# Kernel tuning notes

Measured on AMD Instinct MI355X. Metric: run time of the kernel, lower is better.

## Reference

```python
import jax, jax.numpy as jnp
import numpy as np

HEAD_NUM = 16
ROPE_BASE = 10000.0


def _rotate_half(x):
    # interleaved pairs: (x0,x1,x2,x3,...) -> (-x1,x0,-x3,x2,...)
    x_even = x[..., ::2]
    x_odd = x[..., 1::2]
    return jnp.stack((-x_odd, x_even), axis=-1).reshape(x.shape)


def _rope_cos_sin(seq_len, head_dim):
    half = head_dim // 2
    inv_freq = 1.0 / (ROPE_BASE ** (jnp.arange(half, dtype=jnp.float32) / half))
    t = jnp.arange(seq_len, dtype=jnp.float32)
    freqs = t[:, None] * inv_freq[None, :]            # [S, half]
    cos = jnp.repeat(jnp.cos(freqs), 2, axis=-1)       # [S, D]
    sin = jnp.repeat(jnp.sin(freqs), 2, axis=-1)       # [S, D]
    return cos, sin


def setup_inputs() -> dict:
    key = jax.random.key(0)
    ks = jax.random.split(key, 9)
    B, S, H = 2, 2048, 2048
    std = 1.0 / np.sqrt(H)
    return {
        "x": jax.random.normal(ks[0], (B, S, H), jnp.float32),
        "Wq": jax.random.normal(ks[1], (H, H), jnp.float32) * std,
        "bq": jax.random.normal(ks[2], (H,), jnp.float32) * std,
        "Wk": jax.random.normal(ks[3], (H, H), jnp.float32) * std,
        "bk": jax.random.normal(ks[4], (H,), jnp.float32) * std,
        "Wv": jax.random.normal(ks[5], (H, H), jnp.float32) * std,
        "bv": jax.random.normal(ks[6], (H,), jnp.float32) * std,
        "Wo": jax.random.normal(ks[7], (H, H), jnp.float32) * std,
        "bo": jax.random.normal(ks[8], (H,), jnp.float32) * std,
    }


def reference(x, Wq, bq, Wk, bk, Wv, bv, Wo, bo):
    B, S, H = x.shape
    nh = HEAD_NUM
    d = H // nh
    scale = jnp.float32(np.sqrt(d))

    def proj(W, b):
        y = x @ W.T + b                                 # torch Linear: x W^T + b
        return y.reshape(B, S, nh, d).transpose(0, 2, 1, 3)  # [B, nh, S, d]

    Q = proj(Wq, bq)
    K = proj(Wk, bk)
    V = proj(Wv, bv)

    cos, sin = _rope_cos_sin(S, d)                      # [S, d]
    Q = Q * cos + _rotate_half(Q) * sin
    K = K * cos + _rotate_half(K) * sin

    scores = jnp.einsum("bhqd,bhkd->bhqk", Q, K) / scale  # [B, nh, S, S]
    causal = jnp.tril(jnp.ones((S, S), dtype=bool))
    scores = jnp.where(causal, scores, jnp.float32(-jnp.inf))
    attn = jax.nn.softmax(scores, axis=-1)
    out = jnp.einsum("bhqk,bhkd->bhqd", attn, V)        # [B, nh, S, d]
    out = out.transpose(0, 2, 1, 3).reshape(B, S, H)
    return out @ Wo.T + bo
```

## Files before the change

kernel.cpp:

```cpp
#include <hip/hip_runtime.h>
#include <math.h>

typedef __bf16 bf16x8 __attribute__((ext_vector_type(8)));
typedef float floatx4 __attribute__((ext_vector_type(4)));

__device__ __forceinline__ unsigned short f32_to_bf16(float f) {
  unsigned int u = __float_as_uint(f);
  u = u + 0x7FFFu + ((u >> 16) & 1u);
  return (unsigned short)(u >> 16);
}
__device__ __forceinline__ float bf16_to_f32(unsigned short s) {
  return __uint_as_float(((unsigned int)s) << 16);
}

__device__ __forceinline__ void gld_lds16(const unsigned short* g,
                                          unsigned short* l) {
  __builtin_amdgcn_global_load_lds(
      (const __attribute__((address_space(1))) unsigned int*)g,
      (__attribute__((address_space(3))) unsigned int*)l, 16, 0, 0);
}

__global__ void cast_kernel(const float* __restrict__ in,
                            unsigned short* __restrict__ out, int n4) {
  int i = blockIdx.x * blockDim.x + threadIdx.x;
  if (i >= n4) return;
  const float4 v = reinterpret_cast<const float4*>(in)[i];
  ushort4 o;
  o.x = f32_to_bf16(v.x); o.y = f32_to_bf16(v.y);
  o.z = f32_to_bf16(v.z); o.w = f32_to_bf16(v.w);
  reinterpret_cast<ushort4*>(out)[i] = o;
}

__global__ void cast4_kernel(const float* __restrict__ a,
                             const float* __restrict__ b,
                             const float* __restrict__ c,
                             const float* __restrict__ d,
                             unsigned short* __restrict__ oa,
                             unsigned short* __restrict__ ob,
                             unsigned short* __restrict__ oc,
                             unsigned short* __restrict__ od, int n4) {
  int i = blockIdx.x * blockDim.x + threadIdx.x;
  if (i >= n4) return;
  const float* in;
  unsigned short* out;
  switch (blockIdx.y) {
    case 0: in = a; out = oa; break;
    case 1: in = b; out = ob; break;
    case 2: in = c; out = oc; break;
    default: in = d; out = od; break;
  }
  const float4 v = reinterpret_cast<const float4*>(in)[i];
  ushort4 o;
  o.x = f32_to_bf16(v.x); o.y = f32_to_bf16(v.y);
  o.z = f32_to_bf16(v.z); o.w = f32_to_bf16(v.w);
  reinterpret_cast<ushort4*>(out)[i] = o;
}

__global__ void rope_table_kernel(float2* __restrict__ tab, int total) {
  int idx = blockIdx.x * blockDim.x + threadIdx.x;
  if (idx >= total) return;
  const int s = idx >> 6, i = idx & 63;
  const float inv = powf(10000.0f, -(float)i * (1.0f / 64.0f));
  const float ang = (float)s * inv;
  tab[idx] = make_float2(cosf(ang), sinf(ang));
}

template <int EPI>
__global__ __launch_bounds__(256) void gemm_fused(
    const unsigned short* __restrict__ A, const unsigned short* __restrict__ B,
    const float* __restrict__ bias, float* __restrict__ Cf,
    unsigned short* __restrict__ Cb, const float2* __restrict__ tab,
    float scl, int M, int N, int K, int S) {
  __shared__ unsigned short As[128 * 64];
  __shared__ unsigned short Bs[128 * 64];
  const int t = threadIdx.x;
  const int lane = t & 63;
  const int w = t >> 6;
  const int bm = blockIdx.y * 128;
  const int bn = blockIdx.x * 128;
  const int wm = (w & 1) * 64;
  const int wn = (w >> 1) * 64;
  const int m16 = lane & 15;
  const int quad = lane >> 4;
  const int key = m16 & 7;

  const int lr = lane >> 3;
  const int lc = ((lane & 7) ^ lr) * 8;

  floatx4 acc[4][4];
#pragma unroll
  for (int i = 0; i < 4; ++i)
#pragma unroll
    for (int j = 0; j < 4; ++j) acc[i][j] = floatx4{0.f, 0.f, 0.f, 0.f};

  const unsigned short* Abase = A + (size_t)(bm + w * 32 + lr) * K + lc;
  const unsigned short* Bbase = B + (size_t)(bn + w * 32 + lr) * K + lc;

  for (int k0 = 0; k0 < K; k0 += 64) {
    __syncthreads();
#pragma unroll
    for (int it = 0; it < 4; ++it) {
      gld_lds16(Abase + (size_t)it * 8 * K + k0, &As[(w * 4 + it) * 512]);
      gld_lds16(Bbase + (size_t)it * 8 * K + k0, &Bs[(w * 4 + it) * 512]);
    }
    __syncthreads();
#pragma unroll
    for (int ks = 0; ks < 64; ks += 32) {
      const int ck = ks >> 3;
      bf16x8 af[4], bfr[4];
#pragma unroll
      for (int i = 0; i < 4; ++i)
        af[i] = *reinterpret_cast<const bf16x8*>(
            &As[(wm + i * 16 + m16) * 64 + ((ck | quad) ^ key) * 8]);
#pragma unroll
      for (int j = 0; j < 4; ++j)
        bfr[j] = *reinterpret_cast<const bf16x8*>(
            &Bs[(wn + j * 16 + m16) * 64 + ((ck | quad) ^ key) * 8]);
#pragma unroll
      for (int i = 0; i < 4; ++i)
#pragma unroll
        for (int j = 0; j < 4; ++j)
          acc[i][j] = __builtin_amdgcn_mfma_f32_16x16x32_bf16(
              af[i], bfr[j], acc[i][j], 0, 0, 0);
    }
  }

#pragma unroll
  for (int i = 0; i < 4; ++i) {
    const int rbase = bm + wm + i * 16 + quad * 4;
#pragma unroll
    for (int j = 0; j < 4; ++j) {
      const int col = bn + wn + j * 16 + m16;
      const float bvv = bias[col];
      if (EPI == 0) {
#pragma unroll
        for (int r = 0; r < 4; ++r)
          Cf[(size_t)(rbase + r) * N + col] = acc[i][j][r] + bvv;
      }
    }
  }
}

__global__ __launch_bounds__(256) void gemm_qkv(
    const unsigned short* __restrict__ A, const unsigned short* __restrict__ Bq,
    const unsigned short* __restrict__ Bk, const unsigned short* __restrict__ Bv,
    const float* __restrict__ biasq, const float* __restrict__ biask,
    const float* __restrict__ biasv, unsigned short* __restrict__ Qb,
    unsigned short* __restrict__ Kb, unsigned short* __restrict__ Vtb,
    const float2* __restrict__ tab, float qscale, int M, int N, int K, int S) {
  __shared__ unsigned short As[128 * 64];
  __shared__ unsigned short Bs[128 * 64];
  const int t = threadIdx.x;
  const int lane = t & 63;
  const int w = t >> 6;
  const int z = blockIdx.z;
  const int bm = blockIdx.y * 128;
  const int bn = blockIdx.x * 128;
  const int wm = (w & 1) * 64;
  const int wn = (w >> 1) * 64;
  const int m16 = lane & 15;
  const int quad = lane >> 4;
  const int key = m16 & 7;

  const int lr = lane >> 3;
  const int lc = ((lane & 7) ^ lr) * 8;

  const unsigned short* B = (z == 0) ? Bq : ((z == 1) ? Bk : Bv);
  const float* bias = (z == 0) ? biasq : ((z == 1) ? biask : biasv);
  unsigned short* Cb = (z == 0) ? Qb : ((z == 1) ? Kb : Vtb);
  const float scl = (z == 0) ? qscale : 1.0f;

  floatx4 acc[4][4];
#pragma unroll
  for (int i = 0; i < 4; ++i)
#pragma unroll
    for (int j = 0; j < 4; ++j) acc[i][j] = floatx4{0.f, 0.f, 0.f, 0.f};

  const unsigned short* Abase = A + (size_t)(bm + w * 32 + lr) * K + lc;
  const unsigned short* Bbase = B + (size_t)(bn + w * 32 + lr) * K + lc;

  for (int k0 = 0; k0 < K; k0 += 64) {
    __syncthreads();
#pragma unroll
    for (int it = 0; it < 4; ++it) {
      gld_lds16(Abase + (size_t)it * 8 * K + k0, &As[(w * 4 + it) * 512]);
      gld_lds16(Bbase + (size_t)it * 8 * K + k0, &Bs[(w * 4 + it) * 512]);
    }
    __syncthreads();
#pragma unroll
    for (int ks = 0; ks < 64; ks += 32) {
      const int ck = ks >> 3;
      bf16x8 af[4], bfr[4];
#pragma unroll
      for (int i = 0; i < 4; ++i)
        af[i] = *reinterpret_cast<const bf16x8*>(
            &As[(wm + i * 16 + m16) * 64 + ((ck | quad) ^ key) * 8]);
#pragma unroll
      for (int j = 0; j < 4; ++j)
        bfr[j] = *reinterpret_cast<const bf16x8*>(
            &Bs[(wn + j * 16 + m16) * 64 + ((ck | quad) ^ key) * 8]);
#pragma unroll
      for (int i = 0; i < 4; ++i)
#pragma unroll
        for (int j = 0; j < 4; ++j)
          acc[i][j] = __builtin_amdgcn_mfma_f32_16x16x32_bf16(
              af[i], bfr[j], acc[i][j], 0, 0, 0);
    }
  }

#pragma unroll
  for (int i = 0; i < 4; ++i) {
    const int rbase = bm + wm + i * 16 + quad * 4;
#pragma unroll
    for (int j = 0; j < 4; ++j) {
      const int col = bn + wn + j * 16 + m16;
      const float bvv = bias[col];
      if (z != 2) {
        const int pi = (col & 127) >> 1;
#pragma unroll
        for (int r = 0; r < 4; ++r) {
          const int row = rbase + r;
          const int s = row & (S - 1);
          const float v = acc[i][j][r] + bvv;
          const float vp = __shfl_xor(v, 1);
          const float2 cs = tab[s * 64 + pi];
          const float oe = (v * cs.x - vp * cs.y) * scl;
          const float oo = (vp * cs.x + v * cs.y) * scl;
          if ((m16 & 1) == 0) {
            const unsigned pk =
                (unsigned)f32_to_bf16(oe) | ((unsigned)f32_to_bf16(oo) << 16);
            *reinterpret_cast<unsigned*>(Cb + (size_t)row * N + col) = pk;
          }
        }
      } else {
        const int b = rbase >> 11;
        const int s = rbase & (S - 1);
        ushort4 pk;
        pk.x = f32_to_bf16(acc[i][j][0] + bvv);
        pk.y = f32_to_bf16(acc[i][j][1] + bvv);
        pk.z = f32_to_bf16(acc[i][j][2] + bvv);
        pk.w = f32_to_bf16(acc[i][j][3] + bvv);
        *reinterpret_cast<ushort4*>(
            Cb + ((size_t)((b << 11) + col)) * S + s) = pk;
      }
    }
  }
}

constexpr int F_BQ = 128, F_BK = 64, F_DH = 128;
constexpr int KS_STR = 136;
constexpr int VS_STR = 72;
constexpr int PS_STR = 72;

__global__ __launch_bounds__(256, 2) void fattn_kernel(
    const unsigned short* __restrict__ Qb, const unsigned short* __restrict__ Kb,
    const unsigned short* __restrict__ Vtb, unsigned short* __restrict__ Ob,
    int S, int H, int nh) {
  __shared__ unsigned short Ks[F_BK * KS_STR];
  __shared__ unsigned short Vts[F_DH * VS_STR];
  __shared__ unsigned short Ps[F_BQ * PS_STR];

  const int t = threadIdx.x;
  const int lane = t & 63;
  const int w = t >> 6;
  const int l15 = lane & 15;
  const int quad = lane >> 4;

  const int i = blockIdx.x;
  const int bh = i & 31;
  const int qt = (i < 256) ? (i >> 5) : (15 - ((i - 256) >> 5));
  const int h = bh & 15;
  const int b = bh >> 4;
  const int q0 = qt * F_BQ;

  const unsigned short* Qrow = Qb + ((size_t)(b * S + q0)) * H + h * F_DH;
  const unsigned short* Krow = Kb + ((size_t)b * S) * H + h * F_DH;
  const unsigned short* Vtrow = Vtb + ((size_t)bh * F_DH) * S;
  unsigned short* Orow = Ob + ((size_t)(b * S + q0)) * H + h * F_DH;

  const int kt = t >> 2, ck0 = (t & 3) * 32;
  const int vd = t >> 1, cv0 = (t & 1) * 32;
  const unsigned short* Kg = Krow + (size_t)kt * H + ck0;
  const unsigned short* Vg = Vtrow + (size_t)vd * S + cv0;

  bf16x8 aq[2][4];
#pragma unroll
  for (int qg = 0; qg < 2; ++qg)
#pragma unroll
    for (int ks = 0; ks < 4; ++ks)
      aq[qg][ks] = *reinterpret_cast<const bf16x8*>(
          Qrow + (size_t)(w * 32 + qg * 16 + l15) * H + ks * 32 + quad * 8);

  uint4 kreg[4], vreg[4];
#pragma unroll
  for (int ii = 0; ii < 4; ++ii)
    kreg[ii] = *reinterpret_cast<const uint4*>(Kg + ii * 8);
#pragma unroll
  for (int ii = 0; ii < 4; ++ii)
    vreg[ii] = *reinterpret_cast<const uint4*>(Vg + ii * 8);

  floatx4 oacc[2][8];
#pragma unroll
  for (int qg = 0; qg < 2; ++qg)
#pragma unroll
    for (int dj = 0; dj < 8; ++dj) oacc[qg][dj] = floatx4{0.f, 0.f, 0.f, 0.f};
  float lpart[2][4] = {{0.f, 0.f, 0.f, 0.f}, {0.f, 0.f, 0.f, 0.f}};
  int qrow[2][4];
#pragma unroll
  for (int qg = 0; qg < 2; ++qg)
#pragma unroll
    for (int r = 0; r < 4; ++r)
      qrow[qg][r] = q0 + w * 32 + qg * 16 + quad * 4 + r;

  const int ntile = q0 / F_BK + 2;
  for (int tile = 0; tile < ntile; ++tile) {
    const int k0 = tile * F_BK;
    __syncthreads();
#pragma unroll
    for (int ii = 0; ii < 4; ++ii)
      *reinterpret_cast<uint4*>(&Ks[kt * KS_STR + ck0 + ii * 8]) = kreg[ii];
#pragma unroll
    for (int ii = 0; ii < 4; ++ii)
      *reinterpret_cast<uint4*>(&Vts[vd * VS_STR + cv0 + ii * 8]) = vreg[ii];
    __syncthreads();

    if (tile + 1 < ntile) {
      const int k1 = (tile + 1) * F_BK;
#pragma unroll
      for (int ii = 0; ii < 4; ++ii)
        kreg[ii] = *reinterpret_cast<const uint4*>(Kg + (size_t)k1 * H + ii * 8);
#pragma unroll
      for (int ii = 0; ii < 4; ++ii)
        vreg[ii] = *reinterpret_cast<const uint4*>(Vg + k1 + ii * 8);
    }

    floatx4 sacc[2][4];
#pragma unroll
    for (int qg = 0; qg < 2; ++qg)
#pragma unroll
      for (int j = 0; j < 4; ++j) sacc[qg][j] = floatx4{0.f, 0.f, 0.f, 0.f};
#pragma unroll
    for (int j = 0; j < 4; ++j) {
      bf16x8 bk[4];
#pragma unroll
      for (int ks = 0; ks < 4; ++ks)
        bk[ks] = *reinterpret_cast<const bf16x8*>(
            &Ks[(j * 16 + l15) * KS_STR + ks * 32 + quad * 8]);
#pragma unroll
      for (int qg = 0; qg < 2; ++qg)
#pragma unroll
        for (int ks = 0; ks < 4; ++ks)
          sacc[qg][j] = __builtin_amdgcn_mfma_f32_16x16x32_bf16(
              aq[qg][ks], bk[ks], sacc[qg][j], 0, 0, 0);
    }

#pragma unroll
    for (int qg = 0; qg < 2; ++qg)
#pragma unroll
      for (int j = 0; j < 4; ++j) {
        const int ktg = k0 + j * 16 + l15;
#pragma unroll
        for (int r = 0; r < 4; ++r) {
          const float p =
              (ktg <= qrow[qg][r]) ? exp2f(sacc[qg][j][r]) : 0.0f;
          lpart[qg][r] += p;
          Ps[(w * 32 + qg * 16 + quad * 4 + r) * PS_STR + j * 16 + l15] =
              f32_to_bf16(p);
        }
      }

#pragma unroll
    for (int ks2 = 0; ks2 < 2; ++ks2) {
      bf16x8 ap[2];
#pragma unroll
      for (int qg = 0; qg < 2; ++qg)
        ap[qg] = *reinterpret_cast<const bf16x8*>(
            &Ps[(w * 32 + qg * 16 + l15) * PS_STR + ks2 * 32 + quad * 8]);
#pragma unroll
      for (int dj = 0; dj < 8; ++dj) {
        const bf16x8 bv = *reinterpret_cast<const bf16x8*>(
            &Vts[(dj * 16 + l15) * VS_STR + ks2 * 32 + quad * 8]);
#pragma unroll
        for (int qg = 0; qg < 2; ++qg)
          oacc[qg][dj] = __builtin_amdgcn_mfma_f32_16x16x32_bf16(
              ap[qg], bv, oacc[qg][dj], 0, 0, 0);
      }
    }
  }

#pragma unroll
  for (int qg = 0; qg < 2; ++qg)
#pragma unroll
    for (int r = 0; r < 4; ++r) {
      float l = lpart[qg][r];
      l += __shfl_xor(l, 1);
      l += __shfl_xor(l, 2);
      l += __shfl_xor(l, 4);
      l += __shfl_xor(l, 8);
      const float linv = 1.0f / l;
      unsigned short* orow =
          Orow + (size_t)(w * 32 + qg * 16 + quad * 4 + r) * H;
#pragma unroll
      for (int dj = 0; dj < 8; ++dj)
        orow[dj * 16 + l15] = f32_to_bf16(oacc[qg][dj][r] * linv);
    }
}

extern "C" void kernel_launch(void* const* d_in, const int* in_sizes, int n_in,
                              void* d_out, int out_size, void* d_ws,
                              size_t ws_size, hipStream_t stream) {
  const float* x  = (const float*)d_in[0];
  const float* Wq = (const float*)d_in[1];
  const float* bq = (const float*)d_in[2];
  const float* Wk = (const float*)d_in[3];
  const float* bk = (const float*)d_in[4];
  const float* Wv = (const float*)d_in[5];
  const float* bv = (const float*)d_in[6];
  const float* Wo = (const float*)d_in[7];
  const float* bo = (const float*)d_in[8];
  float* out = (float*)d_out;

  const int B = 2, S = 2048, H = 2048, nh = 16;
  const int M = B * S;

  unsigned short* Wqb = (unsigned short*)d_ws;
  unsigned short* Wkb = Wqb + (size_t)H * H;
  unsigned short* Wvb = Wkb + (size_t)H * H;
  unsigned short* Wob = Wvb + (size_t)H * H;
  unsigned short* xb  = Wob + (size_t)H * H;
  unsigned short* Qbb = xb + (size_t)M * H;
  unsigned short* Kbb = Qbb + (size_t)M * H;
  unsigned short* Vtb = Kbb + (size_t)M * H;
  unsigned short* Ob  = Vtb + (size_t)M * H;
  float2* tab = (float2*)(Ob + (size_t)M * H);

  const int cast_w4 = H * H / 4;
  const int cast_x4 = M * H / 4;
  const int tab_n = S * 64;

  rope_table_kernel<<<dim3(tab_n / 256), dim3(256), 0, stream>>>(tab, tab_n);
  cast_kernel<<<dim3(cast_x4 / 256), dim3(256), 0, stream>>>(x, xb, cast_x4);
  cast4_kernel<<<dim3(cast_w4 / 256, 4), dim3(256), 0, stream>>>(
      Wq, Wk, Wv, Wo, Wqb, Wkb, Wvb, Wob, cast_w4);

  const float qscale = 0.08838834764831845f * 1.4426950408889634f;

  gemm_qkv<<<dim3(H / 128, M / 128, 3), dim3(256), 0, stream>>>(
      xb, Wqb, Wkb, Wvb, bq, bk, bv, Qbb, Kbb, Vtb, tab, qscale, M, H, H, S);

  fattn_kernel<<<dim3((S / F_BQ) * B * nh), dim3(256), 0, stream>>>(
      Qbb, Kbb, Vtb, Ob, S, H, nh);

  gemm_fused<0><<<dim3(H / 128, M / 128), dim3(256), 0, stream>>>(
      Ob, Wob, bo, out, nullptr, nullptr, 1.0f, M, H, H, S);
}
```

Baseline: 473.3 us.

## Swizzle GEMM workgroup order and drop register prefetch in flash attention

Both GEMM kernels remap the linear workgroup id in groups of 8, interleaving blocks across a stride of nwg/8, so that concurrently running workgroups are intended to share A/B tiles in L2/MALL. The attention kernel removes the software prefetch of the next K/V tile into registers and instead loads each tile synchronously from global memory into LDS at the start of its iteration. This lowers register pressure and may allow higher occupancy, but global load latency is no longer hidden behind the MFMA work of the previous tile. A bias variable is also renamed.

```diff
diff --git a/kernel.cpp b/kernel.cpp
--- a/kernel.cpp
+++ b/kernel.cpp
@@ -76,8 +76,13 @@
   const int t = threadIdx.x;
   const int lane = t & 63;
   const int w = t >> 6;
-  const int bm = blockIdx.y * 128;
-  const int bn = blockIdx.x * 128;
+
+  const int nwg = gridDim.x * gridDim.y;
+  const int orig = blockIdx.y * gridDim.x + blockIdx.x;
+  const int wgid = (orig & 7) * (nwg >> 3) + (orig >> 3);
+  const int bm = (wgid / gridDim.x) * 128;
+  const int bn = (wgid % gridDim.x) * 128;
+
   const int wm = (w & 1) * 64;
   const int wn = (w >> 1) * 64;
   const int m16 = lane & 15;
@@ -131,11 +136,11 @@
 #pragma unroll
     for (int j = 0; j < 4; ++j) {
       const int col = bn + wn + j * 16 + m16;
-      const float bvv = bias[col];
+      const float bv = bias[col];
       if (EPI == 0) {
 #pragma unroll
         for (int r = 0; r < 4; ++r)
-          Cf[(size_t)(rbase + r) * N + col] = acc[i][j][r] + bvv;
+          Cf[(size_t)(rbase + r) * N + col] = acc[i][j][r] + bv;
       }
     }
   }
@@ -154,8 +159,13 @@
   const int lane = t & 63;
   const int w = t >> 6;
   const int z = blockIdx.z;
-  const int bm = blockIdx.y * 128;
-  const int bn = blockIdx.x * 128;
+
+  const int nwg = gridDim.x * gridDim.y;
+  const int orig = blockIdx.y * gridDim.x + blockIdx.x;
+  const int wgid = (orig & 7) * (nwg >> 3) + (orig >> 3);
+  const int bm = (wgid / gridDim.x) * 128;
+  const int bn = (wgid % gridDim.x) * 128;
+
   const int wm = (w & 1) * 64;
   const int wn = (w >> 1) * 64;
   const int m16 = lane & 15;
@@ -278,11 +288,6 @@
   const unsigned short* Vtrow = Vtb + ((size_t)bh * F_DH) * S;
   unsigned short* Orow = Ob + ((size_t)(b * S + q0)) * H + h * F_DH;
 
-  const int kt = t >> 2, ck0 = (t & 3) * 32;
-  const int vd = t >> 1, cv0 = (t & 1) * 32;
-  const unsigned short* Kg = Krow + (size_t)kt * H + ck0;
-  const unsigned short* Vg = Vtrow + (size_t)vd * S + cv0;
-
   bf16x8 aq[2][4];
 #pragma unroll
   for (int qg = 0; qg < 2; ++qg)
@@ -291,14 +296,6 @@
       aq[qg][ks] = *reinterpret_cast<const bf16x8*>(
           Qrow + (size_t)(w * 32 + qg * 16 + l15) * H + ks * 32 + quad * 8);
 
-  uint4 kreg[4], vreg[4];
-#pragma unroll
-  for (int ii = 0; ii < 4; ++ii)
-    kreg[ii] = *reinterpret_cast<const uint4*>(Kg + ii * 8);
-#pragma unroll
-  for (int ii = 0; ii < 4; ++ii)
-    vreg[ii] = *reinterpret_cast<const uint4*>(Vg + ii * 8);
-
   floatx4 oacc[2][8];
 #pragma unroll
   for (int qg = 0; qg < 2; ++qg)
@@ -316,23 +313,23 @@
   for (int tile = 0; tile < ntile; ++tile) {
     const int k0 = tile * F_BK;
     __syncthreads();
-#pragma unroll
-    for (int ii = 0; ii < 4; ++ii)
-      *reinterpret_cast<uint4*>(&Ks[kt * KS_STR + ck0 + ii * 8]) = kreg[ii];
-#pragma unroll
-    for (int ii = 0; ii < 4; ++ii)
-      *reinterpret_cast<uint4*>(&Vts[vd * VS_STR + cv0 + ii * 8]) = vreg[ii];
-    __syncthreads();
-
-    if (tile + 1 < ntile) {
-      const int k1 = (tile + 1) * F_BK;
+    {
+      const int kt = t >> 2, c0 = (t & 3) * 32;
+      const unsigned short* g = Krow + (size_t)(k0 + kt) * H + c0;
 #pragma unroll
       for (int ii = 0; ii < 4; ++ii)
-        kreg[ii] = *reinterpret_cast<const uint4*>(Kg + (size_t)k1 * H + ii * 8);
+        *reinterpret_cast<uint4*>(&Ks[kt * KS_STR + c0 + ii * 8]) =
+            *reinterpret_cast<const uint4*>(g + ii * 8);
+    }
+    {
+      const int d = t >> 1, c0 = (t & 1) * 32;
+      const unsigned short* g = Vtrow + (size_t)d * S + k0 + c0;
 #pragma unroll
       for (int ii = 0; ii < 4; ++ii)
-        vreg[ii] = *reinterpret_cast<const uint4*>(Vg + k1 + ii * 8);
-    }
+        *reinterpret_cast<uint4*>(&Vts[d * VS_STR + c0 + ii * 8]) =
+            *reinterpret_cast<const uint4*>(g + ii * 8);
+    }
+    __syncthreads();
 
     floatx4 sacc[2][4];
 #pragma unroll
```

Measured after the change: 408.3 us. 1.16x faster.
